# Performance work log

Hardware: AMD Instinct MI355X
Metric: run time of the kernel (lower is better)

Reference implementation:

```python
import jax, jax.numpy as jnp
import numpy as np

H = 16  # heads (query_heads == kv_heads in this config)
LN_EPS = 1e-5


def setup_inputs() -> dict:
    key = jax.random.key(0)
    ks = jax.random.split(key, 6)
    B, T, C = 4, 1024, 1024
    s = lambda fan_in: 1.0 / np.sqrt(fan_in)
    return {
        "x": jax.random.normal(ks[0], (B, T, C), jnp.float32),
        "c_attn_w": jax.random.normal(ks[1], (C, 3 * C), jnp.float32) * s(C),
        "c_attn_b": jnp.zeros((3 * C,), jnp.float32),
        "q_w": jax.random.normal(ks[2], (C, C), jnp.float32) * s(C),
        "q_b": jnp.zeros((C,), jnp.float32),
        "k_w": jax.random.normal(ks[3], (C, C), jnp.float32) * s(C),
        "k_b": jnp.zeros((C,), jnp.float32),
        "v_w": jax.random.normal(ks[4], (C, C), jnp.float32) * s(C),
        "v_b": jnp.zeros((C,), jnp.float32),
        "ln_g": jnp.ones((C,), jnp.float32),
        "ln_b": jnp.zeros((C,), jnp.float32),
        "out_w": jax.random.normal(ks[5], (C, C), jnp.float32) * s(C),
        "out_b": jnp.zeros((C,), jnp.float32),
    }


def reference(x, c_attn_w, c_attn_b, q_w, q_b, k_w, k_b, v_w, v_b,
              ln_g, ln_b, out_w, out_b):
    B, T, C = x.shape
    d = C // H
    # c_attn then split into query/key/value streams
    qkv = x @ c_attn_w + c_attn_b            # [B,T,3C]
    query, key_, value = jnp.split(qkv, 3, axis=-1)
    q = query @ q_w + q_b                     # [B,T,C]
    k = key_ @ k_w + k_b
    v = value @ v_w + v_b
    # split heads: b n (h d) -> b h n d
    q = q.reshape(B, T, H, d).transpose(0, 2, 1, 3)
    k = k.reshape(B, T, H, d).transpose(0, 2, 1, 3)
    v = v.reshape(B, T, H, d).transpose(0, 2, 1, 3)
    scale = d ** 0.5
    # NOTE: original code scales query by 1/scale AND the similarity by 1/scale
    # (net 1/d). Preserved faithfully.
    sim = jnp.einsum("bhnd,bhsd->bhns", q / scale, k)  # [B,H,T,T]
    causal = jnp.tril(jnp.ones((T, T), dtype=bool))
    sim = jnp.where(causal, sim, jnp.finfo(sim.dtype).min)
    attn = jax.nn.softmax(sim / scale, axis=-1)
    o = jnp.einsum("bhns,bhsd->bnhd", attn, v).reshape(B, T, C)
    # LayerNorm (eps=1e-5)
    mu = jnp.mean(o, axis=-1, keepdims=True)
    var = jnp.var(o, axis=-1, keepdims=True)
    o = (o - mu) * jax.lax.rsqrt(var + LN_EPS) * ln_g + ln_b
    return o @ out_w + out_b
```

## Files before the change

### kernel.cpp

```cpp
#include <hip/hip_runtime.h>
#include <hip/hip_bf16.h>
#include <stdint.h>

typedef __bf16 bf16_t;
typedef bf16_t bf16x4 __attribute__((ext_vector_type(4)));
typedef bf16_t bf16x8 __attribute__((ext_vector_type(8)));
typedef float  f32x4  __attribute__((ext_vector_type(4)));

#define B_   4
#define T_   1024
#define C_   1024
#define H_   16

__device__ __forceinline__ f32x4 mfma_bf16(bf16x8 a, bf16x8 b, f32x4 c) {
  return __builtin_amdgcn_mfma_f32_16x16x32_bf16(a, b, c, 0, 0, 0);
}

__device__ __forceinline__ void async16(const bf16_t* g, bf16_t* l) {
  __builtin_amdgcn_global_load_lds(
      (__attribute__((address_space(1))) void*)(uintptr_t)g,
      (__attribute__((address_space(3))) void*)l, 16, 0, 0);
}

__global__ __launch_bounds__(256) void convert_f32_bf16(
    const float* __restrict__ in, bf16_t* __restrict__ out, int n4)
{
  const int i = blockIdx.x * 256 + threadIdx.x;
  if (i >= n4) return;
  const float4 v = *(const float4*)(in + (size_t)i * 4);
  bf16x4 o;
  o[0] = (bf16_t)v.x; o[1] = (bf16_t)v.y; o[2] = (bf16_t)v.z; o[3] = (bf16_t)v.w;
  *(bf16x4*)(out + (size_t)i * 4) = o;
}

__global__ __launch_bounds__(256) void transpose4_f32_bf16(
    const float* __restrict__ a0, const float* __restrict__ a1,
    const float* __restrict__ a2, const float* __restrict__ a3,
    bf16_t* __restrict__ out)
{
  __shared__ bf16_t tile[32][33];
  const int z = blockIdx.z;
  const float* in = (z == 0) ? a0 : (z == 1) ? a1 : (z == 2) ? a2 : a3;
  bf16_t* o = out + ((size_t)z << 20);
  const int n0 = blockIdx.x * 32, k0 = blockIdx.y * 32;
  const int x = threadIdx.x & 31, y4 = (threadIdx.x >> 5) * 4;
#pragma unroll
  for (int i = 0; i < 4; ++i)
    tile[y4 + i][x] = (bf16_t)in[(size_t)(k0 + y4 + i) * 1024 + n0 + x];
  __syncthreads();
#pragma unroll
  for (int i = 0; i < 4; ++i)
    o[(size_t)(n0 + y4 + i) * 1024 + k0 + x] = tile[x][y4 + i];
}

__global__ __launch_bounds__(256) void transpose_v(
    const bf16_t* __restrict__ qkvb, bf16_t* __restrict__ vfrag)
{
  __shared__ bf16_t tile[64][66];
  const int bid = blockIdx.x;
  const int kb = bid & 15, bh = bid >> 4;
  const int b = bh >> 4, h = bh & 15;
  const int t = threadIdx.x;
  {
    const int key = t & 63, fc = (t >> 6) * 16;
    const bf16_t* src =
        qkvb + (size_t)(b * 1024 + kb * 64 + key) * 3072 + 2048 + h * 64 + fc;
    bf16x8 v0 = *(const bf16x8*)src;
    bf16x8 v1 = *(const bf16x8*)(src + 8);
#pragma unroll
    for (int j = 0; j < 8; ++j) {
      tile[fc + j][key]     = v0[j];
      tile[fc + 8 + j][key] = v1[j];
    }
  }
  __syncthreads();
#pragma unroll
  for (int ww = 0; ww < 2; ++ww) {
    const int g = t * 2 + ww;
    const int chunk = g >> 6;
    const int lane2 = g & 63;
    const int lr2 = lane2 & 15, lg2 = lane2 >> 4;
    const int kk = chunk >> 2, nf = chunk & 3;
    const int f = nf * 16 + lr2;
    const int key0 = kk * 32 + lg2 * 8;
    bf16x8 val;
#pragma unroll
    for (int j = 0; j < 8; ++j) val[j] = tile[f][key0 + j];
    *(bf16x8*)&vfrag[(((size_t)bh * 16 + kb) * 8 + chunk) * 512 + lane2 * 8] = val;
  }
}

__global__ __launch_bounds__(256) void bias_eff_kernel(
    const float* __restrict__ cb,
    const float* __restrict__ w0, const float* __restrict__ w1,
    const float* __restrict__ w2,
    const float* __restrict__ b0, const float* __restrict__ b1,
    const float* __restrict__ b2,
    float* __restrict__ out)
{
  __shared__ float part[4][64];
  const int j0 = blockIdx.x * 64;
  const int jl = threadIdx.x & 63, cq = threadIdx.x >> 6;
  const int j = j0 + jl;
  const int s = j >> 10, jj = j & 1023;
  const float* w  = (s == 0) ? w0 : (s == 1) ? w1 : w2;
  const float* sb = (s == 0) ? b0 : (s == 1) ? b1 : b2;
  float acc = 0.f;
  const int c0 = cq * 256;
#pragma unroll 8
  for (int c = c0; c < c0 + 256; ++c)
    acc += cb[s * 1024 + c] * w[(size_t)c * 1024 + jj];
  part[cq][jl] = acc;
  __syncthreads();
  if (cq == 0)
    out[j] = part[0][jl] + part[1][jl] + part[2][jl] + part[3][jl] + sb[jj];
}

template <typename OT>
__global__ __launch_bounds__(256) void gemm_bt_bias(
    const bf16_t* __restrict__ A, int lda,
    const bf16_t* __restrict__ Bt, int ldb,
    const float* __restrict__ bias,
    OT* __restrict__ C, int ldc,
    int K, int nTilesN, int blocksPerMat,
    int strideA, int strideB, int strideC, int xcdSwz)
{
  __shared__ __align__(16) bf16_t As[3][128 * 32];
  __shared__ __align__(16) bf16_t Bs[3][128 * 32];
  int raw = blockIdx.x;
  if (xcdSwz) {
    const int cpx = gridDim.x >> 3;
    raw = (raw & 7) * cpx + (raw >> 3);
  }
  const int s   = raw / blocksPerMat;
  const int bid = raw % blocksPerMat;
  A  += (size_t)s * strideA;
  Bt += (size_t)s * strideB;
  C  += (size_t)s * strideC;
  const int mt = bid / nTilesN, nt = bid % nTilesN;
  const int m0 = mt * 128, n0 = nt * 128;
  const int tid = threadIdx.x;
  const int lane = tid & 63;
  const int lr = lane & 15, lg = lane >> 4;
  const int wid = tid >> 6;
  const int wr = wid >> 1, wc = wid & 1;
  const int sLg = lg ^ ((lr >> 1) & 3);

  f32x4 acc[4][4];
#pragma unroll
  for (int m = 0; m < 4; ++m)
#pragma unroll
    for (int n = 0; n < 4; ++n) acc[m][n] = (f32x4){0.f, 0.f, 0.f, 0.f};

  const int nk = K >> 5;

  auto stage = [&](int buf, int t) {
    const int k0 = t << 5;
#pragma unroll
    for (int p = 0; p < 2; ++p) {
      const int c = p * 256 + tid;
      const int row = c >> 2;
      const int col = (((c & 3) ^ ((c >> 3) & 3)) << 3);
      async16(A + (size_t)(m0 + row) * lda + k0 + col, &As[buf][c * 8]);
      async16(Bt + (size_t)(n0 + row) * ldb + k0 + col, &Bs[buf][c * 8]);
    }
  };

  stage(0, 0);
  stage(1, 1);
  asm volatile("s_waitcnt vmcnt(4)" ::: "memory");
  __builtin_amdgcn_sched_barrier(0);
  __builtin_amdgcn_s_barrier();
  __builtin_amdgcn_sched_barrier(0);

  for (int t = 0; t < nk; ++t) {
    const int buf = t % 3;
    if (t + 2 < nk) stage((t + 2) % 3, t + 2);

    bf16x8 af[4], bfr[4];
#pragma unroll
    for (int m = 0; m < 4; ++m)
      af[m] = *(const bf16x8*)&As[buf][(wr * 64 + m * 16 + lr) * 32 + sLg * 8];
#pragma unroll
    for (int n = 0; n < 4; ++n)
      bfr[n] = *(const bf16x8*)&Bs[buf][(wc * 64 + n * 16 + lr) * 32 + sLg * 8];

    if (t + 2 < nk)
      asm volatile("s_waitcnt lgkmcnt(0) vmcnt(4)" ::: "memory");
    else
      asm volatile("s_waitcnt lgkmcnt(0) vmcnt(0)" ::: "memory");
    __builtin_amdgcn_sched_barrier(0);
    __builtin_amdgcn_s_barrier();
    __builtin_amdgcn_sched_barrier(0);

    __builtin_amdgcn_s_setprio(1);
#pragma unroll
    for (int m = 0; m < 4; ++m)
#pragma unroll
      for (int n = 0; n < 4; ++n)
        acc[m][n] = mfma_bf16(af[m], bfr[n], acc[m][n]);
    __builtin_amdgcn_s_setprio(0);
  }

#pragma unroll
  for (int n = 0; n < 4; ++n) {
    const int col = n0 + wc * 64 + n * 16 + lr;
    const float bv = bias ? bias[col] : 0.0f;
#pragma unroll
    for (int m = 0; m < 4; ++m) {
      const int row = m0 + wr * 64 + m * 16 + lg * 4;
#pragma unroll
      for (int r = 0; r < 4; ++r)
        C[(size_t)(row + r) * ldc + col] = (OT)(acc[m][n][r] + bv);
    }
  }
}

__global__ __launch_bounds__(256) void attn_kernel(
    const bf16_t* __restrict__ qkv, const bf16_t* __restrict__ vfrag,
    bf16_t* __restrict__ o)
{
  __shared__ __align__(16) bf16_t Ks[2][8][512];
  __shared__ __align__(16) bf16_t Vs[2][8][512];
  __shared__ __align__(16) bf16_t Ps[4][16][72];
  const int LD = 3072;
  const bf16_t* q = qkv;
  const bf16_t* k = qkv + 1024;

  const int raw = blockIdx.x;
  const int xcd = raw & 7, idx = raw >> 3;
  const int bh   = (idx >> 3) * 8 + xcd;
  const int slot = idx & 7;
  const int b = bh >> 4, h = bh & 15;

  const int tid = threadIdx.x;
  const int lane = tid & 63;
  const int lr = lane & 15, lg = lane >> 4;
  const int w = tid >> 6;

  const bf16_t* kbase = k + (size_t)(b * T_) * LD + h * 64;
  const bf16_t* vfbase = vfrag + (size_t)bh * 16 * 8 * 512;

  auto stage = [&](int bf, int it) {
    const int kv0 = it << 6;
#pragma unroll
    for (int cc = 0; cc < 4; ++cc) {
      const int c = w * 4 + cc;
      if (c < 8) {
        const int kg = c >> 1, kk = c & 1;
        async16(kbase + (size_t)(kv0 + kg * 16 + lr) * LD + kk * 32 + lg * 8,
                &Ks[bf][c][lane * 8]);
      } else {
        const int cv = c - 8;
        async16(vfbase + ((size_t)it * 8 + cv) * 512 + lane * 8,
                &Vs[bf][cv][lane * 8]);
      }
    }
  };

#pragma unroll
  for (int pass = 0; pass < 2; ++pass) {
    const int band = pass ? (15 - slot) : slot;
    const int myq = band * 64 + w * 16 + lr;
    const int nIter = band + 1;

    bf16x8 qf[2];
    {
      const size_t qr = (size_t)(b * T_ + myq) * LD + h * 64;
      qf[0] = *(const bf16x8*)&q[qr + lg * 8];
      qf[1] = *(const bf16x8*)&q[qr + 32 + lg * 8];
    }

    float mi = -3.0e38f, li = 0.0f;
    f32x4 acc[4];
#pragma unroll
    for (int nf = 0; nf < 4; ++nf) acc[nf] = (f32x4){0.f, 0.f, 0.f, 0.f};

    stage(0, 0);
    __syncthreads();

    for (int it = 0; it < nIter; ++it) {
      const int bf = it & 1;
      if (it + 1 < nIter) stage(bf ^ 1, it + 1);
      const int kv0 = it << 6;

      f32x4 sfr[4];
      __builtin_amdgcn_s_setprio(1);
#pragma unroll
      for (int kg = 0; kg < 4; ++kg) {
        bf16x8 kf0 = *(const bf16x8*)&Ks[bf][kg * 2 + 0][lane * 8];
        bf16x8 kf1 = *(const bf16x8*)&Ks[bf][kg * 2 + 1][lane * 8];
        f32x4 z = (f32x4){0.f, 0.f, 0.f, 0.f};
        z = mfma_bf16(kf0, qf[0], z);
        z = mfma_bf16(kf1, qf[1], z);
        sfr[kg] = z;
      }
      __builtin_amdgcn_s_setprio(0);

      float sv[4][4];
      float pm[4];
#pragma unroll
      for (int kg = 0; kg < 4; ++kg) {
        const int keyb = kv0 + kg * 16 + lg * 4;
        pm[kg] = -3.0e38f;
#pragma unroll
        for (int r = 0; r < 4; ++r) {
          float xx = sfr[kg][r] * 0.015625f;
          if (keyb + r > myq) xx = -3.0e38f;
          sv[kg][r] = xx;
          pm[kg] = fmaxf(pm[kg], xx);
        }
      }
      float pmax = fmaxf(fmaxf(pm[0], pm[1]), fmaxf(pm[2], pm[3]));
      pmax = fmaxf(pmax, __shfl_xor(pmax, 16));
      pmax = fmaxf(pmax, __shfl_xor(pmax, 32));
      const float mnew = fmaxf(mi, pmax);
      const float fr = __expf(mi - mnew);
      mi = mnew;
      float ps[4];
#pragma unroll
      for (int kg = 0; kg < 4; ++kg) {
        float p0 = __expf(sv[kg][0] - mi);
        float p1 = __expf(sv[kg][1] - mi);
        float p2 = __expf(sv[kg][2] - mi);
        float p3 = __expf(sv[kg][3] - mi);
        sv[kg][0] = p0; sv[kg][1] = p1; sv[kg][2] = p2; sv[kg][3] = p3;
        ps[kg] = (p0 + p1) + (p2 + p3);
      }
      float psum = (ps[0] + ps[1]) + (ps[2] + ps[3]);
      psum += __shfl_xor(psum, 16);
      psum += __shfl_xor(psum, 32);
      li = li * fr + psum;
#pragma unroll
      for (int nf = 0; nf < 4; ++nf)
#pragma unroll
        for (int r = 0; r < 4; ++r) acc[nf][r] *= fr;

#pragma unroll
      for (int kg = 0; kg < 4; ++kg) {
        bf16x4 p4;
#pragma unroll
        for (int r = 0; r < 4; ++r) p4[r] = (bf16_t)sv[kg][r];
        *(bf16x4*)&Ps[w][lr][kg * 16 + lg * 4] = p4;
      }

      __builtin_amdgcn_s_setprio(1);
#pragma unroll
      for (int kk = 0; kk < 2; ++kk) {
        bf16x8 pf = *(const bf16x8*)&Ps[w][lr][kk * 32 + lg * 8];
#pragma unroll
        for (int nf = 0; nf < 4; ++nf) {
          bf16x8 vf = *(const bf16x8*)&Vs[bf][kk * 4 + nf][lane * 8];
          acc[nf] = mfma_bf16(vf, pf, acc[nf]);
        }
      }
      __builtin_amdgcn_s_setprio(0);

      __syncthreads();
    }

    const float inv = 1.0f / li;
#pragma unroll
    for (int nf = 0; nf < 4; ++nf) {
      bf16x4 o4;
#pragma unroll
      for (int r = 0; r < 4; ++r) o4[r] = (bf16_t)(acc[nf][r] * inv);
      *(bf16x4*)&o[(size_t)(b * T_ + myq) * C_ + h * 64 + nf * 16 + lg * 4] = o4;
    }
  }
}

__global__ __launch_bounds__(256) void ln_kernel(
    const bf16_t* __restrict__ in,
    const float* __restrict__ g,
    const float* __restrict__ be,
    bf16_t* __restrict__ out)
{
  const int row = blockIdx.x * 4 + (threadIdx.x >> 6);
  const int lane = threadIdx.x & 63;
  const bf16_t* p = in + (size_t)row * C_ + lane * 16;
  bf16x8 a0 = *(const bf16x8*)p;
  bf16x8 a1 = *(const bf16x8*)(p + 8);
  float xs[16];
#pragma unroll
  for (int j = 0; j < 8; ++j) { xs[j] = (float)a0[j]; xs[8 + j] = (float)a1[j]; }
  float sum = 0.f, sq = 0.f;
#pragma unroll
  for (int j = 0; j < 16; ++j) { sum += xs[j]; sq += xs[j] * xs[j]; }
#pragma unroll
  for (int dd = 1; dd < 64; dd <<= 1) {
    sum += __shfl_xor(sum, dd);
    sq  += __shfl_xor(sq, dd);
  }
  const float mean = sum * (1.0f / 1024.0f);
  const float var  = sq * (1.0f / 1024.0f) - mean * mean;
  const float rstd = rsqrtf(var + 1e-5f);
  float gv[16], bv[16];
#pragma unroll
  for (int j = 0; j < 4; ++j) {
    *(float4*)&gv[j * 4] = *(const float4*)(g  + lane * 16 + j * 4);
    *(float4*)&bv[j * 4] = *(const float4*)(be + lane * 16 + j * 4);
  }
  bf16x8 o0, o1;
#pragma unroll
  for (int j = 0; j < 8; ++j) {
    o0[j] = (bf16_t)((xs[j] - mean) * rstd * gv[j] + bv[j]);
    o1[j] = (bf16_t)((xs[8 + j] - mean) * rstd * gv[8 + j] + bv[8 + j]);
  }
  bf16_t* op = out + (size_t)row * C_ + lane * 16;
  *(bf16x8*)op = o0;
  *(bf16x8*)(op + 8) = o1;
}

extern "C" void kernel_launch(void* const* d_in, const int* in_sizes, int n_in,
                              void* d_out, int out_size, void* d_ws, size_t ws_size,
                              hipStream_t stream)
{
  const float* x        = (const float*)d_in[0];
  const float* c_attn_w = (const float*)d_in[1];
  const float* c_attn_b = (const float*)d_in[2];
  const float* q_w      = (const float*)d_in[3];
  const float* q_b      = (const float*)d_in[4];
  const float* k_w      = (const float*)d_in[5];
  const float* k_b      = (const float*)d_in[6];
  const float* v_w      = (const float*)d_in[7];
  const float* v_b      = (const float*)d_in[8];
  const float* ln_g     = (const float*)d_in[9];
  const float* ln_b     = (const float*)d_in[10];
  const float* out_w    = (const float*)d_in[11];
  const float* out_b    = (const float*)d_in[12];

  char* ws = (char*)d_ws;
  bf16_t* qkvb      = (bf16_t*)(ws + 0);
  bf16_t* xb        = (bf16_t*)(ws + 25165824);
  bf16_t* lnb       = (bf16_t*)(ws + 25165824);
  bf16_t* WsT4      = (bf16_t*)(ws + 33554432);
  bf16_t* c_attn_wb = (bf16_t*)(ws + 41943040);
  bf16_t* Wt_eff    = (bf16_t*)(ws + 48234496);
  float*  bias_eff  = (float*)(ws + 54525952);
  bf16_t* vfrag     = (bf16_t*)(ws + 54538240);

  convert_f32_bf16<<<dim3(4096), 256, 0, stream>>>(x, xb, 1048576);
  convert_f32_bf16<<<dim3(3072), 256, 0, stream>>>(c_attn_w, c_attn_wb, 786432);

  transpose4_f32_bf16<<<dim3(32, 32, 4), 256, 0, stream>>>(
      q_w, k_w, v_w, out_w, WsT4);

  gemm_bt_bias<bf16_t><<<dim3(192), 256, 0, stream>>>(
      WsT4, 1024, c_attn_wb, 3072, nullptr, Wt_eff, 1024,
      1024, 8, 64, 1 << 20, 1024, 1 << 20, 0);

  bias_eff_kernel<<<dim3(48), 256, 0, stream>>>(
      c_attn_b, q_w, k_w, v_w, q_b, k_b, v_b, bias_eff);

  gemm_bt_bias<bf16_t><<<dim3(768), 256, 0, stream>>>(
      xb, 1024, Wt_eff, 1024, bias_eff, qkvb, 3072, 1024, 24, 768, 0, 0, 0, 1);

  transpose_v<<<dim3(1024), 256, 0, stream>>>(qkvb, vfrag);

  attn_kernel<<<dim3(512), 256, 0, stream>>>(qkvb, vfrag, (bf16_t*)d_out);

  ln_kernel<<<dim3(1024), 256, 0, stream>>>((const bf16_t*)d_out, ln_g, ln_b, lnb);

  gemm_bt_bias<float><<<dim3(256), 256, 0, stream>>>(
      lnb, 1024, WsT4 + (size_t)3 * (1 << 20), 1024, out_b,
      (float*)d_out, 1024, 1024, 8, 256, 0, 0, 0, 1);
}
```

Measured before the change: 160.1 us.

## Fold LayerNorm into output GEMM via row statistics and pre-scaled weights

Removes the separate LayerNorm kernel. The attention kernel now accumulates per-row sum and sum-of-squares with atomics, ln_g is folded into the transposed out_w, and the output GEMM epilogue applies mean/rstd correction using precomputed g·W and b·W+out_b vectors. It also merges the two f32→bf16 conversions into one launch and adds the extra vector precomputes to the bias kernel. This saves one kernel launch plus a full read and write of the activation, at the cost of atomics, variance computed as E[x²]−mean² on unnormalized data, and bf16 rounding of unnormalized activations before the GEMM.

```diff
diff --git a/kernel.cpp b/kernel.cpp
--- a/kernel.cpp
+++ b/kernel.cpp
@@ -22,21 +22,25 @@
       (__attribute__((address_space(3))) void*)l, 16, 0, 0);
 }
 
-__global__ __launch_bounds__(256) void convert_f32_bf16(
-    const float* __restrict__ in, bf16_t* __restrict__ out, int n4)
+__global__ __launch_bounds__(256) void convert2_f32_bf16(
+    const float* __restrict__ a, bf16_t* __restrict__ oa, int na4,
+    const float* __restrict__ b, bf16_t* __restrict__ ob, int nb4)
 {
   const int i = blockIdx.x * 256 + threadIdx.x;
-  if (i >= n4) return;
-  const float4 v = *(const float4*)(in + (size_t)i * 4);
+  const float* src; bf16_t* dst; int idx;
+  if (i < na4) { src = a; dst = oa; idx = i; }
+  else if (i < na4 + nb4) { src = b; dst = ob; idx = i - na4; }
+  else return;
+  const float4 v = *(const float4*)(src + (size_t)idx * 4);
   bf16x4 o;
   o[0] = (bf16_t)v.x; o[1] = (bf16_t)v.y; o[2] = (bf16_t)v.z; o[3] = (bf16_t)v.w;
-  *(bf16x4*)(out + (size_t)i * 4) = o;
+  *(bf16x4*)(dst + (size_t)idx * 4) = o;
 }
 
 __global__ __launch_bounds__(256) void transpose4_f32_bf16(
     const float* __restrict__ a0, const float* __restrict__ a1,
     const float* __restrict__ a2, const float* __restrict__ a3,
-    bf16_t* __restrict__ out)
+    const float* __restrict__ lng, bf16_t* __restrict__ out)
 {
   __shared__ bf16_t tile[32][33];
   const int z = blockIdx.z;
@@ -45,8 +49,11 @@
   const int n0 = blockIdx.x * 32, k0 = blockIdx.y * 32;
   const int x = threadIdx.x & 31, y4 = (threadIdx.x >> 5) * 4;
 #pragma unroll
-  for (int i = 0; i < 4; ++i)
-    tile[y4 + i][x] = (bf16_t)in[(size_t)(k0 + y4 + i) * 1024 + n0 + x];
+  for (int i = 0; i < 4; ++i) {
+    float v = in[(size_t)(k0 + y4 + i) * 1024 + n0 + x];
+    if (z == 3) v *= lng[k0 + y4 + i];
+    tile[y4 + i][x] = (bf16_t)v;
+  }
   __syncthreads();
 #pragma unroll
   for (int i = 0; i < 4; ++i)
@@ -90,30 +97,59 @@
   }
 }
 
-__global__ __launch_bounds__(256) void bias_eff_kernel(
+__global__ __launch_bounds__(256) void prep_vec_kernel(
     const float* __restrict__ cb,
     const float* __restrict__ w0, const float* __restrict__ w1,
     const float* __restrict__ w2,
     const float* __restrict__ b0, const float* __restrict__ b1,
     const float* __restrict__ b2,
-    float* __restrict__ out)
-{
+    const float* __restrict__ ow, const float* __restrict__ lng,
+    const float* __restrict__ lnb, const float* __restrict__ outb,
+    float* __restrict__ out_qkv, float* __restrict__ svec,
+    float* __restrict__ c2v, float* __restrict__ ssum, float* __restrict__ ssq)
+{
+  const int bid = blockIdx.x;
+  if (bid >= 80) {
+    const float4 z = {0.f, 0.f, 0.f, 0.f};
+#pragma unroll
+    for (int k = 0; k < 4; ++k) {
+      ((float4*)ssum)[threadIdx.x * 4 + k] = z;
+      ((float4*)ssq)[threadIdx.x * 4 + k] = z;
+    }
+    return;
+  }
   __shared__ float part[4][64];
-  const int j0 = blockIdx.x * 64;
   const int jl = threadIdx.x & 63, cq = threadIdx.x >> 6;
-  const int j = j0 + jl;
-  const int s = j >> 10, jj = j & 1023;
-  const float* w  = (s == 0) ? w0 : (s == 1) ? w1 : w2;
-  const float* sb = (s == 0) ? b0 : (s == 1) ? b1 : b2;
-  float acc = 0.f;
   const int c0 = cq * 256;
+  if (bid < 48) {
+    const int j = bid * 64 + jl;
+    const int s = j >> 10, jj = j & 1023;
+    const float* w  = (s == 0) ? w0 : (s == 1) ? w1 : w2;
+    const float* sb = (s == 0) ? b0 : (s == 1) ? b1 : b2;
+    float acc = 0.f;
 #pragma unroll 8
-  for (int c = c0; c < c0 + 256; ++c)
-    acc += cb[s * 1024 + c] * w[(size_t)c * 1024 + jj];
-  part[cq][jl] = acc;
-  __syncthreads();
-  if (cq == 0)
-    out[j] = part[0][jl] + part[1][jl] + part[2][jl] + part[3][jl] + sb[jj];
+    for (int c = c0; c < c0 + 256; ++c)
+      acc += cb[s * 1024 + c] * w[(size_t)c * 1024 + jj];
+    part[cq][jl] = acc;
+    __syncthreads();
+    if (cq == 0)
+      out_qkv[j] = part[0][jl] + part[1][jl] + part[2][jl] + part[3][jl] + sb[jj];
+  } else {
+    const int jj = (bid - 48) * 64 + jl;
+    const int col = jj & 1023;
+    const float* coef = (jj < 1024) ? lng : lnb;
+    float acc = 0.f;
+#pragma unroll 8
+    for (int c = c0; c < c0 + 256; ++c)
+      acc += coef[c] * ow[(size_t)c * 1024 + col];
+    part[cq][jl] = acc;
+    __syncthreads();
+    if (cq == 0) {
+      const float tot = part[0][jl] + part[1][jl] + part[2][jl] + part[3][jl];
+      if (jj < 1024) svec[col] = tot;
+      else           c2v[col] = tot + outb[col];
+    }
+  }
 }
 
 template <typename OT>
@@ -216,9 +252,109 @@
   }
 }
 
+__global__ __launch_bounds__(256) void gemm_ln(
+    const bf16_t* __restrict__ A, int lda,
+    const bf16_t* __restrict__ Bt, int ldb,
+    const float* __restrict__ svec, const float* __restrict__ c2v,
+    const float* __restrict__ ssum, const float* __restrict__ ssq,
+    float* __restrict__ C, int ldc, int K, int nTilesN)
+{
+  __shared__ __align__(16) bf16_t As[3][128 * 32];
+  __shared__ __align__(16) bf16_t Bs[3][128 * 32];
+  int raw = blockIdx.x;
+  {
+    const int cpx = gridDim.x >> 3;
+    raw = (raw & 7) * cpx + (raw >> 3);
+  }
+  const int mt = raw / nTilesN, nt = raw % nTilesN;
+  const int m0 = mt * 128, n0 = nt * 128;
+  const int tid = threadIdx.x;
+  const int lane = tid & 63;
+  const int lr = lane & 15, lg = lane >> 4;
+  const int wid = tid >> 6;
+  const int wr = wid >> 1, wc = wid & 1;
+  const int sLg = lg ^ ((lr >> 1) & 3);
+
+  f32x4 acc[4][4];
+#pragma unroll
+  for (int m = 0; m < 4; ++m)
+#pragma unroll
+    for (int n = 0; n < 4; ++n) acc[m][n] = (f32x4){0.f, 0.f, 0.f, 0.f};
+
+  const int nk = K >> 5;
+
+  auto stage = [&](int buf, int t) {
+    const int k0 = t << 5;
+#pragma unroll
+    for (int p = 0; p < 2; ++p) {
+      const int c = p * 256 + tid;
+      const int row = c >> 2;
+      const int col = (((c & 3) ^ ((c >> 3) & 3)) << 3);
+      async16(A + (size_t)(m0 + row) * lda + k0 + col, &As[buf][c * 8]);
+      async16(Bt + (size_t)(n0 + row) * ldb + k0 + col, &Bs[buf][c * 8]);
+    }
+  };
+
+  stage(0, 0);
+  stage(1, 1);
+  asm volatile("s_waitcnt vmcnt(4)" ::: "memory");
+  __builtin_amdgcn_sched_barrier(0);
+  __builtin_amdgcn_s_barrier();
+  __builtin_amdgcn_sched_barrier(0);
+
+  for (int t = 0; t < nk; ++t) {
+    const int buf = t % 3;
+    if (t + 2 < nk) stage((t + 2) % 3, t + 2);
+
+    bf16x8 af[4], bfr[4];
+#pragma unroll
+    for (int m = 0; m < 4; ++m)
+      af[m] = *(const bf16x8*)&As[buf][(wr * 64 + m * 16 + lr) * 32 + sLg * 8];
+#pragma unroll
+    for (int n = 0; n < 4; ++n)
+      bfr[n] = *(const bf16x8*)&Bs[buf][(wc * 64 + n * 16 + lr) * 32 + sLg * 8];
+
+    if (t + 2 < nk)
+      asm volatile("s_waitcnt lgkmcnt(0) vmcnt(4)" ::: "memory");
+    else
+      asm volatile("s_waitcnt lgkmcnt(0) vmcnt(0)" ::: "memory");
+    __builtin_amdgcn_sched_barrier(0);
+    __builtin_amdgcn_s_barrier();
+    __builtin_amdgcn_sched_barrier(0);
+
+    __builtin_amdgcn_s_setprio(1);
+#pragma unroll
+    for (int m = 0; m < 4; ++m)
+#pragma unroll
+      for (int n = 0; n < 4; ++n)
+        acc[m][n] = mfma_bf16(af[m], bfr[n], acc[m][n]);
+    __builtin_amdgcn_s_setprio(0);
+  }
+
+#pragma unroll
+  for (int n = 0; n < 4; ++n) {
+    const int col = n0 + wc * 64 + n * 16 + lr;
+    const float sj = svec[col];
+    const float c2 = c2v[col];
+#pragma unroll
+    for (int m = 0; m < 4; ++m) {
+      const int row = m0 + wr * 64 + m * 16 + lg * 4;
+      const float* s1 = &ssum[row];
+      const float* s2 = &ssq[row];
+#pragma unroll
+      for (int r = 0; r < 4; ++r) {
+        const float mu  = s1[r] * (1.0f / 1024.0f);
+        const float var = s2[r] * (1.0f / 1024.0f) - mu * mu;
+        const float al  = rsqrtf(var + 1e-5f);
+        C[(size_t)(row + r) * ldc + col] = al * acc[m][n][r] - al * mu * sj + c2;
+      }
+    }
+  }
+}
+
 __global__ __launch_bounds__(256) void attn_kernel(
     const bf16_t* __restrict__ qkv, const bf16_t* __restrict__ vfrag,
-    bf16_t* __restrict__ o)
+    bf16_t* __restrict__ o, float* __restrict__ ssum, float* __restrict__ ssq)
 {
   __shared__ __align__(16) bf16_t Ks[2][8][512];
   __shared__ __align__(16) bf16_t Vs[2][8][512];
@@ -360,56 +496,26 @@
     }
 
     const float inv = 1.0f / li;
+    float st1 = 0.f, st2 = 0.f;
 #pragma unroll
     for (int nf = 0; nf < 4; ++nf) {
       bf16x4 o4;
 #pragma unroll
-      for (int r = 0; r < 4; ++r) o4[r] = (bf16_t)(acc[nf][r] * inv);
+      for (int r = 0; r < 4; ++r) {
+        const float ov = acc[nf][r] * inv;
+        o4[r] = (bf16_t)ov;
+        st1 += ov;
+        st2 += ov * ov;
+      }
       *(bf16x4*)&o[(size_t)(b * T_ + myq) * C_ + h * 64 + nf * 16 + lg * 4] = o4;
     }
-  }
-}
-
-__global__ __launch_bounds__(256) void ln_kernel(
-    const bf16_t* __restrict__ in,
-    const float* __restrict__ g,
-    const float* __restrict__ be,
-    bf16_t* __restrict__ out)
-{
-  const int row = blockIdx.x * 4 + (threadIdx.x >> 6);
-  const int lane = threadIdx.x & 63;
-  const bf16_t* p = in + (size_t)row * C_ + lane * 16;
-  bf16x8 a0 = *(const bf16x8*)p;
-  bf16x8 a1 = *(const bf16x8*)(p + 8);
-  float xs[16];
-#pragma unroll
-  for (int j = 0; j < 8; ++j) { xs[j] = (float)a0[j]; xs[8 + j] = (float)a1[j]; }
-  float sum = 0.f, sq = 0.f;
-#pragma unroll
-  for (int j = 0; j < 16; ++j) { sum += xs[j]; sq += xs[j] * xs[j]; }
-#pragma unroll
-  for (int dd = 1; dd < 64; dd <<= 1) {
-    sum += __shfl_xor(sum, dd);
-    sq  += __shfl_xor(sq, dd);
-  }
-  const float mean = sum * (1.0f / 1024.0f);
-  const float var  = sq * (1.0f / 1024.0f) - mean * mean;
-  const float rstd = rsqrtf(var + 1e-5f);
-  float gv[16], bv[16];
-#pragma unroll
-  for (int j = 0; j < 4; ++j) {
-    *(float4*)&gv[j * 4] = *(const float4*)(g  + lane * 16 + j * 4);
-    *(float4*)&bv[j * 4] = *(const float4*)(be + lane * 16 + j * 4);
-  }
-  bf16x8 o0, o1;
-#pragma unroll
-  for (int j = 0; j < 8; ++j) {
-    o0[j] = (bf16_t)((xs[j] - mean) * rstd * gv[j] + bv[j]);
-    o1[j] = (bf16_t)((xs[8 + j] - mean) * rstd * gv[8 + j] + bv[8 + j]);
-  }
-  bf16_t* op = out + (size_t)row * C_ + lane * 16;
-  *(bf16x8*)op = o0;
-  *(bf16x8*)(op + 8) = o1;
+    st1 += __shfl_xor(st1, 16); st1 += __shfl_xor(st1, 32);
+    st2 += __shfl_xor(st2, 16); st2 += __shfl_xor(st2, 32);
+    if (lg == 0) {
+      atomicAdd(&ssum[b * T_ + myq], st1);
+      atomicAdd(&ssq[b * T_ + myq], st2);
+    }
+  }
 }
 
 extern "C" void kernel_launch(void* const* d_in, const int* in_sizes, int n_in,
@@ -433,36 +539,39 @@
   char* ws = (char*)d_ws;
   bf16_t* qkvb      = (bf16_t*)(ws + 0);
   bf16_t* xb        = (bf16_t*)(ws + 25165824);
-  bf16_t* lnb       = (bf16_t*)(ws + 25165824);
+  bf16_t* ob        = (bf16_t*)(ws + 25165824);
   bf16_t* WsT4      = (bf16_t*)(ws + 33554432);
   bf16_t* c_attn_wb = (bf16_t*)(ws + 41943040);
   bf16_t* Wt_eff    = (bf16_t*)(ws + 48234496);
   float*  bias_eff  = (float*)(ws + 54525952);
   bf16_t* vfrag     = (bf16_t*)(ws + 54538240);
-
-  convert_f32_bf16<<<dim3(4096), 256, 0, stream>>>(x, xb, 1048576);
-  convert_f32_bf16<<<dim3(3072), 256, 0, stream>>>(c_attn_w, c_attn_wb, 786432);
+  float*  ssum      = (float*)(ws + 62926848);
+  float*  ssq       = (float*)(ws + 62943232);
+  float*  svec      = (float*)(ws + 62959616);
+  float*  c2v       = (float*)(ws + 62963712);
+
+  convert2_f32_bf16<<<dim3(7168), 256, 0, stream>>>(
+      x, xb, 1048576, c_attn_w, c_attn_wb, 786432);
 
   transpose4_f32_bf16<<<dim3(32, 32, 4), 256, 0, stream>>>(
-      q_w, k_w, v_w, out_w, WsT4);
+      q_w, k_w, v_w, out_w, ln_g, WsT4);
 
   gemm_bt_bias<bf16_t><<<dim3(192), 256, 0, stream>>>(
       WsT4, 1024, c_attn_wb, 3072, nullptr, Wt_eff, 1024,
       1024, 8, 64, 1 << 20, 1024, 1 << 20, 0);
 
-  bias_eff_kernel<<<dim3(48), 256, 0, stream>>>(
-      c_attn_b, q_w, k_w, v_w, q_b, k_b, v_b, bias_eff);
+  prep_vec_kernel<<<dim3(81), 256, 0, stream>>>(
+      c_attn_b, q_w, k_w, v_w, q_b, k_b, v_b,
+      out_w, ln_g, ln_b, out_b, bias_eff, svec, c2v, ssum, ssq);
 
   gemm_bt_bias<bf16_t><<<dim3(768), 256, 0, stream>>>(
       xb, 1024, Wt_eff, 1024, bias_eff, qkvb, 3072, 1024, 24, 768, 0, 0, 0, 1);
 
   transpose_v<<<dim3(1024), 256, 0, stream>>>(qkvb, vfrag);
 
-  attn_kernel<<<dim3(512), 256, 0, stream>>>(qkvb, vfrag, (bf16_t*)d_out);
-
-  ln_kernel<<<dim3(1024), 256, 0, stream>>>((const bf16_t*)d_out, ln_g, ln_b, lnb);
-
-  gemm_bt_bias<float><<<dim3(256), 256, 0, stream>>>(
-      lnb, 1024, WsT4 + (size_t)3 * (1 << 20), 1024, out_b,
-      (float*)d_out, 1024, 1024, 8, 256, 0, 0, 0, 1);
-}
+  attn_kernel<<<dim3(512), 256, 0, stream>>>(qkvb, vfrag, ob, ssum, ssq);
+
+  gemm_ln<<<dim3(256), 256, 0, stream>>>(
+      ob, 1024, WsT4 + (size_t)3 * (1 << 20), 1024,
+      svec, c2v, ssum, ssq, (float*)d_out, 1024, 1024, 8);
+}
```

New measurement: 154.0 us. 1.04x faster.
